# Performance work log

Measured on AMD Instinct MI355X. Metric: run time of the kernel, lower is better.

Reference implementation:

```python
import jax, jax.numpy as jnp
import numpy as np

B = 262144
P = 0.8
CLS_NUM_LIST = [500, 477, 456, 435, 415, 396, 378, 361, 345, 329, 314, 300, 286, 273, 261, 249, 238, 227, 217, 207, 197, 188, 180, 172, 164, 156, 149, 142, 136, 130, 124, 118, 113, 108, 103, 98, 94, 90, 85, 82, 78, 74, 71, 68, 65, 62, 59, 56, 54, 51, 49, 47, 45, 43, 41, 39, 37, 35, 34, 32, 31, 29, 28, 27, 26, 24, 23, 22, 21, 20, 19, 18, 18, 17, 16, 15, 15, 14, 13, 13, 12, 12, 11, 11, 10, 10, 9, 9, 8, 8, 8, 7, 7, 7, 6, 6, 6, 5, 5, 5]
C = len(CLS_NUM_LIST)


def _build_weight_matrix():
    n = np.asarray(CLS_NUM_LIST, dtype=np.float64).reshape(C, 1)
    wm = (1.0 / n) * n.T            # wm[i, j] = n_j / n_i
    wm[wm > 1] = 1.0
    wm = np.power(wm, P)
    return jnp.asarray(wm, dtype=jnp.float32)


def setup_inputs() -> dict:
    key = jax.random.key(0)
    kx, kt = jax.random.split(key)
    x = jax.random.normal(kx, (B, C), dtype=jnp.float32)
    target = jax.random.randint(kt, (B,), 0, C, dtype=jnp.int64)
    weight_matrix = _build_weight_matrix()                      # [C, C]
    neg_grad = jnp.full((1, C), 1e-06, dtype=jnp.float32)
    pos_grad = jnp.full((1, C), 1e-06, dtype=jnp.float32)
    return {"x": x, "target": target, "weight_matrix": weight_matrix,
            "neg_grad": neg_grad, "pos_grad": pos_grad}


def reference(x, target, weight_matrix, neg_grad, pos_grad):
    bs, num_classes = x.shape
    onehot = jax.nn.one_hot(target, num_classes, dtype=x.dtype)   # [B, C]
    # one_hot @ weight_matrix is algebraically a row gather
    weight = weight_matrix[target]                                # [B, C]
    weighted_x = x + jnp.log(weight)
    log_sm = jax.nn.log_softmax(weighted_x, axis=1)               # stable log(softmax)
    softmax_x = jnp.exp(log_sm)
    # grad-statistic accumulation (detached in the original)
    grad = jnp.abs(softmax_x - onehot)
    neg_grad_new = neg_grad + (grad * (1.0 - onehot)).sum(0)      # [1, C]
    pos_grad_new = pos_grad + (grad * onehot).sum(0)              # [1, C]
    ratio = pos_grad_new / neg_grad_new
    loss = -jnp.sum(onehot * log_sm) / bs
    return loss, neg_grad_new, pos_grad_new, ratio
```

## Files before the change

### kernel.cpp

```cpp
#include <hip/hip_runtime.h>

#define NCLS 100
#define NROWS 262144
#define MAIN_BLOCKS 2048
#define MAIN_THREADS 256
#define NWAVES (MAIN_THREADS / 64)
#define NOCT ((MAIN_BLOCKS * MAIN_THREADS) / 8)
#define ROWS_PER_OCT (NROWS / NOCT)
#define PART_LD MAIN_BLOCKS
#define NPC (2 * NCLS + 1)
#define WS_NEEDED ((size_t)NPC * PART_LD * 4)


#define LOADX(buf, rp) do {                                                    \
    buf[0] = (rp)[k];                                                          \
    buf[1] = (rp)[8 + k];                                                      \
    buf[2] = (rp)[16 + k];                                                     \
    buf[3] = (k == 0) ? (rp)[24] : make_float4(0.f, 0.f, 0.f, 0.f);            \
} while (0)

#define COMPROW(buf, LGT, VTX, TT) do {                                        \
    float4 e[4];                                                               \
    float sp = 0.f;                                                            \
    _Pragma("unroll")                                                          \
    for (int m = 0; m < 4; ++m) {                                              \
        if (8 * m + k < 25) {                                                  \
            e[m].x = __expf(buf[m].x + fminf(lgn[m].x - (LGT), 0.f));          \
            e[m].y = __expf(buf[m].y + fminf(lgn[m].y - (LGT), 0.f));          \
            e[m].z = __expf(buf[m].z + fminf(lgn[m].z - (LGT), 0.f));          \
            e[m].w = __expf(buf[m].w + fminf(lgn[m].w - (LGT), 0.f));          \
            sp += (e[m].x + e[m].y) + (e[m].z + e[m].w);                       \
        } else {                                                               \
            e[m] = make_float4(0.f, 0.f, 0.f, 0.f);                            \
        }                                                                      \
    }                                                                          \
    float s = sp + __shfl_xor(sp, 1, 64);                                      \
    s += __shfl_xor(s, 2, 64);                                                 \
    s += __shfl_xor(s, 4, 64);                                                 \
    const float inv_s = 1.0f / s;                                              \
    if (k == 0) {                                                              \
        loss_local += __logf(s) - (VTX);                                       \
        const float pt = __expf(VTX) * inv_s;                                  \
        atomicAdd(&lds_q[TT], pt);                                             \
        atomicAdd(&lds_pos[TT], 1.0f - pt);                                    \
    }                                                                          \
    _Pragma("unroll")                                                          \
    for (int m = 0; m < 4; ++m) {                                              \
        if (8 * m + k < 25) {                                                  \
            S4[m].x = fmaf(e[m].x, inv_s, S4[m].x);                            \
            S4[m].y = fmaf(e[m].y, inv_s, S4[m].y);                            \
            S4[m].z = fmaf(e[m].z, inv_s, S4[m].z);                            \
            S4[m].w = fmaf(e[m].w, inv_s, S4[m].w);                            \
        }                                                                      \
    }                                                                          \
} while (0)

__global__ __launch_bounds__(MAIN_THREADS, 4)
void seesaw_main(const float* __restrict__ x,
                 const int* __restrict__ target,
                 const float* __restrict__ wm,
                 float* __restrict__ part,
                 float* __restrict__ out,
                 int use_part) {
    __shared__ float lds_lgn[NCLS];
    __shared__ float lds_q[NCLS];
    __shared__ float lds_pos[NCLS];
    __shared__ float lds_S[NWAVES][NCLS];
    __shared__ float lds_loss[NWAVES];

    const int lane = threadIdx.x & 63;
    const int wave = threadIdx.x >> 6;
    const int k    = threadIdx.x & 7;
    const int oct  = (blockIdx.x * MAIN_THREADS + threadIdx.x) >> 3;

    int tr[ROWS_PER_OCT];
#pragma unroll
    for (int r = 0; r < ROWS_PER_OCT; ++r) tr[r] = target[oct + r * NOCT];

    if (threadIdx.x < NCLS) {
        lds_lgn[threadIdx.x] = __logf(wm[threadIdx.x]);
        lds_q[threadIdx.x] = 0.f;
        lds_pos[threadIdx.x] = 0.f;
    }
    __syncthreads();

    float vtx[ROWS_PER_OCT], lgt[ROWS_PER_OCT];
    const float4* xr[ROWS_PER_OCT];
#pragma unroll
    for (int r = 0; r < ROWS_PER_OCT; ++r) {
        const int row = oct + r * NOCT;
        xr[r] = reinterpret_cast<const float4*>(x + (size_t)row * NCLS);
        vtx[r] = x[(size_t)row * NCLS + tr[r]];
    }

    float4 lgn[4];
#pragma unroll
    for (int m = 0; m < 4; ++m) {
        const int g = 8 * m + k;
        if (g < 25) {
            lgn[m].x = lds_lgn[4 * g + 0];
            lgn[m].y = lds_lgn[4 * g + 1];
            lgn[m].z = lds_lgn[4 * g + 2];
            lgn[m].w = lds_lgn[4 * g + 3];
        } else {
            lgn[m] = make_float4(0.f, 0.f, 0.f, 0.f);
        }
    }
#pragma unroll
    for (int r = 0; r < ROWS_PER_OCT; ++r) lgt[r] = lds_lgn[tr[r]];

    float4 S4[4];
#pragma unroll
    for (int m = 0; m < 4; ++m) S4[m] = make_float4(0.f, 0.f, 0.f, 0.f);
    float loss_local = 0.0f;

    float4 xv0[4], xv1[4], xv2[4];
    LOADX(xv0, xr[0]);
    LOADX(xv1, xr[1]);
    LOADX(xv2, xr[2]);
    COMPROW(xv0, lgt[0], vtx[0], tr[0]);
    LOADX(xv0, xr[3]);
    COMPROW(xv1, lgt[1], vtx[1], tr[1]);
    COMPROW(xv2, lgt[2], vtx[2], tr[2]);
    COMPROW(xv0, lgt[3], vtx[3], tr[3]);

#pragma unroll
    for (int m = 0; m < 4; ++m) {
#pragma unroll
        for (int msk = 8; msk <= 32; msk <<= 1) {
            S4[m].x += __shfl_xor(S4[m].x, msk, 64);
            S4[m].y += __shfl_xor(S4[m].y, msk, 64);
            S4[m].z += __shfl_xor(S4[m].z, msk, 64);
            S4[m].w += __shfl_xor(S4[m].w, msk, 64);
        }
    }
#pragma unroll
    for (int msk = 1; msk < 64; msk <<= 1)
        loss_local += __shfl_xor(loss_local, msk, 64);
    if (lane == 0) lds_loss[wave] = loss_local;

    if (lane < 8) {
#pragma unroll
        for (int m = 0; m < 4; ++m) {
            const int g = 8 * m + lane;
            if (g < 25) {
                lds_S[wave][4 * g + 0] = S4[m].x;
                lds_S[wave][4 * g + 1] = S4[m].y;
                lds_S[wave][4 * g + 2] = S4[m].z;
                lds_S[wave][4 * g + 3] = S4[m].w;
            }
        }
    }
    __syncthreads();

    if (use_part) {
        if (threadIdx.x < NCLS) {
            const int j = threadIdx.x;
            float sb = 0.f;
#pragma unroll
            for (int w = 0; w < NWAVES; ++w) sb += lds_S[w][j];
            part[(size_t)j * PART_LD + blockIdx.x] = sb - lds_q[j];
            part[(size_t)(NCLS + j) * PART_LD + blockIdx.x] = lds_pos[j];
        }
        if (threadIdx.x == 0) {
            float l = 0.f;
#pragma unroll
            for (int w = 0; w < NWAVES; ++w) l += lds_loss[w];
            part[(size_t)(2 * NCLS) * PART_LD + blockIdx.x] = l;
        }
    } else {
        if (threadIdx.x < NCLS) {
            const int j = threadIdx.x;
            float sb = 0.f;
#pragma unroll
            for (int w = 0; w < NWAVES; ++w) sb += lds_S[w][j];
            atomicAdd(&out[1 + j], sb - lds_q[j]);
            atomicAdd(&out[1 + NCLS + j], lds_pos[j]);
        }
        if (threadIdx.x == 0) {
            float l = 0.f;
#pragma unroll
            for (int w = 0; w < NWAVES; ++w) l += lds_loss[w];
            atomicAdd(&out[0], l);
        }
    }
}

__global__ void seesaw_tail(const float* __restrict__ part,
                            const float* __restrict__ neg_in,
                            const float* __restrict__ pos_in,
                            float* __restrict__ out) {
    const int c = blockIdx.x;
    __shared__ float redn[NWAVES], redp[NWAVES];
    const int lane = threadIdx.x & 63;
    const int wave = threadIdx.x >> 6;

    float sn = 0.f, sp = 0.f;
    if (c < NCLS) {
        for (int b = threadIdx.x; b < PART_LD; b += MAIN_THREADS) {
            sn += part[(size_t)c * PART_LD + b];
            sp += part[(size_t)(NCLS + c) * PART_LD + b];
        }
    } else {
        for (int b = threadIdx.x; b < PART_LD; b += MAIN_THREADS)
            sn += part[(size_t)(2 * NCLS) * PART_LD + b];
    }
#pragma unroll
    for (int msk = 1; msk < 64; msk <<= 1) {
        sn += __shfl_xor(sn, msk, 64);
        sp += __shfl_xor(sp, msk, 64);
    }
    if (lane == 0) { redn[wave] = sn; redp[wave] = sp; }
    __syncthreads();
    if (threadIdx.x == 0) {
        float tn = 0.f, tp = 0.f;
#pragma unroll
        for (int w = 0; w < NWAVES; ++w) { tn += redn[w]; tp += redp[w]; }
        if (c < NCLS) {
            const float neg = neg_in[c] + tn;
            const float pos = pos_in[c] + tp;
            out[1 + c] = neg;
            out[1 + NCLS + c] = pos;
            out[1 + 2 * NCLS + c] = pos / neg;
        } else {
            out[0] = tn * (1.0f / (float)NROWS);
        }
    }
}

__global__ void seesaw_init(const float* __restrict__ neg_in,
                            const float* __restrict__ pos_in,
                            float* __restrict__ out) {
    int i = threadIdx.x;
    if (i == 0) out[0] = 0.0f;
    if (i < NCLS) {
        out[1 + i] = neg_in[i];
        out[1 + NCLS + i] = pos_in[i];
    }
}

__global__ void seesaw_fin(float* __restrict__ out) {
    int j = threadIdx.x;
    if (j == 0) out[0] *= (1.0f / (float)NROWS);
    if (j < NCLS) out[1 + 2 * NCLS + j] = out[1 + NCLS + j] / out[1 + j];
}

extern "C" void kernel_launch(void* const* d_in, const int* in_sizes, int n_in,
                              void* d_out, int out_size, void* d_ws, size_t ws_size,
                              hipStream_t stream) {
    const float* x      = (const float*)d_in[0];
    const int*   target = (const int*)d_in[1];
    const float* wm     = (const float*)d_in[2];
    const float* neg_in = (const float*)d_in[3];
    const float* pos_in = (const float*)d_in[4];
    float* out  = (float*)d_out;
    float* part = (float*)d_ws;

    if (ws_size >= WS_NEEDED) {
        hipLaunchKernelGGL(seesaw_main, dim3(MAIN_BLOCKS), dim3(MAIN_THREADS), 0, stream,
                           x, target, wm, part, out, 1);
        hipLaunchKernelGGL(seesaw_tail, dim3(NCLS + 1), dim3(MAIN_THREADS), 0, stream,
                           part, neg_in, pos_in, out);
    } else {
        hipLaunchKernelGGL(seesaw_init, dim3(1), dim3(256), 0, stream,
                           neg_in, pos_in, out);
        hipLaunchKernelGGL(seesaw_main, dim3(MAIN_BLOCKS), dim3(MAIN_THREADS), 0, stream,
                           x, target, wm, part, out, 0);
        hipLaunchKernelGGL(seesaw_fin, dim3(1), dim3(128), 0, stream, out);
    }
}
```

Before: 31.91 us.

## Stage contiguous x tiles through LDS with coalesced loads per block

Each block now owns a contiguous chunk of 128 rows. It copies them into LDS one 32-row tile at a time using fully coalesced float4 loads, then computes each row from LDS. The target-logit gather also reads from LDS instead of making a scattered global load. This is meant to replace strided per-octet row reads and the extra global gather, at the cost of serialising load and compute with block-wide barriers, so memory latency is no longer overlapped with compute within the block.

Measured after the change: 36.17 us. +13.3%, slower.

```diff
diff --git a/kernel.cpp b/kernel.cpp
--- a/kernel.cpp
+++ b/kernel.cpp
@@ -5,19 +5,13 @@
 #define MAIN_BLOCKS 2048
 #define MAIN_THREADS 256
 #define NWAVES (MAIN_THREADS / 64)
-#define NOCT ((MAIN_BLOCKS * MAIN_THREADS) / 8)
-#define ROWS_PER_OCT (NROWS / NOCT)
+#define TILE_ROWS 32
+#define NTILES 4
+#define TILE_F4 (TILE_ROWS * 25)
 #define PART_LD MAIN_BLOCKS
 #define NPC (2 * NCLS + 1)
 #define WS_NEEDED ((size_t)NPC * PART_LD * 4)
 
-
-#define LOADX(buf, rp) do {                                                    \
-    buf[0] = (rp)[k];                                                          \
-    buf[1] = (rp)[8 + k];                                                      \
-    buf[2] = (rp)[16 + k];                                                     \
-    buf[3] = (k == 0) ? (rp)[24] : make_float4(0.f, 0.f, 0.f, 0.f);            \
-} while (0)
 
 #define COMPROW(buf, LGT, VTX, TT) do {                                        \
     float4 e[4];                                                               \
@@ -55,6 +49,28 @@
     }                                                                          \
 } while (0)
 
+#define STAGE(TI) do {                                                         \
+    _Pragma("unroll")                                                          \
+    for (int i_ = 0; i_ < 4; ++i_) {                                           \
+        const int idx_ = i_ * MAIN_THREADS + threadIdx.x;                      \
+        if (idx_ < TILE_F4)                                                    \
+            lds_x4[idx_] = x4[base_f4 + (TI) * TILE_F4 + idx_];                \
+    }                                                                          \
+} while (0)
+
+#define COMPTILE(TI) do {                                                      \
+    const int t_ = tr[TI];                                                     \
+    const float lgt_ = lgt[TI];                                                \
+    float4 buf[4];                                                             \
+    buf[0] = lds_x4[oct * 25 + k];                                             \
+    buf[1] = lds_x4[oct * 25 + 8 + k];                                         \
+    buf[2] = lds_x4[oct * 25 + 16 + k];                                        \
+    buf[3] = (k == 0) ? lds_x4[oct * 25 + 24]                                  \
+                      : make_float4(0.f, 0.f, 0.f, 0.f);                       \
+    const float vt_ = lds_xs[oct * NCLS + t_];   \
+    COMPROW(buf, lgt_, vt_, t_);                                               \
+} while (0)
+
 __global__ __launch_bounds__(MAIN_THREADS, 4)
 void seesaw_main(const float* __restrict__ x,
                  const int* __restrict__ target,
@@ -62,6 +78,7 @@
                  float* __restrict__ part,
                  float* __restrict__ out,
                  int use_part) {
+    __shared__ float4 lds_x4[TILE_F4];
     __shared__ float lds_lgn[NCLS];
     __shared__ float lds_q[NCLS];
     __shared__ float lds_pos[NCLS];
@@ -71,27 +88,25 @@
     const int lane = threadIdx.x & 63;
     const int wave = threadIdx.x >> 6;
     const int k    = threadIdx.x & 7;
-    const int oct  = (blockIdx.x * MAIN_THREADS + threadIdx.x) >> 3;
-
-    int tr[ROWS_PER_OCT];
-#pragma unroll
-    for (int r = 0; r < ROWS_PER_OCT; ++r) tr[r] = target[oct + r * NOCT];
+    const int oct  = threadIdx.x >> 3;
+    const float* lds_xs = reinterpret_cast<const float*>(lds_x4);
+    const float4* x4 = reinterpret_cast<const float4*>(x);
+    const size_t base_f4 = (size_t)blockIdx.x * (NTILES * TILE_F4);
+    const int row0 = blockIdx.x * (NTILES * TILE_ROWS) + oct;
+
+    int tr[NTILES];
+    tr[0] = target[row0];
+    tr[1] = target[row0 + TILE_ROWS];
+    tr[2] = target[row0 + 2 * TILE_ROWS];
+    tr[3] = target[row0 + 3 * TILE_ROWS];
 
     if (threadIdx.x < NCLS) {
         lds_lgn[threadIdx.x] = __logf(wm[threadIdx.x]);
         lds_q[threadIdx.x] = 0.f;
         lds_pos[threadIdx.x] = 0.f;
     }
-    __syncthreads();
-
-    float vtx[ROWS_PER_OCT], lgt[ROWS_PER_OCT];
-    const float4* xr[ROWS_PER_OCT];
-#pragma unroll
-    for (int r = 0; r < ROWS_PER_OCT; ++r) {
-        const int row = oct + r * NOCT;
-        xr[r] = reinterpret_cast<const float4*>(x + (size_t)row * NCLS);
-        vtx[r] = x[(size_t)row * NCLS + tr[r]];
-    }
+    STAGE(0);
+    __syncthreads();
 
     float4 lgn[4];
 #pragma unroll
@@ -106,23 +121,30 @@
             lgn[m] = make_float4(0.f, 0.f, 0.f, 0.f);
         }
     }
-#pragma unroll
-    for (int r = 0; r < ROWS_PER_OCT; ++r) lgt[r] = lds_lgn[tr[r]];
+    float lgt[NTILES];
+    lgt[0] = lds_lgn[tr[0]];
+    lgt[1] = lds_lgn[tr[1]];
+    lgt[2] = lds_lgn[tr[2]];
+    lgt[3] = lds_lgn[tr[3]];
 
     float4 S4[4];
 #pragma unroll
     for (int m = 0; m < 4; ++m) S4[m] = make_float4(0.f, 0.f, 0.f, 0.f);
     float loss_local = 0.0f;
 
-    float4 xv0[4], xv1[4], xv2[4];
-    LOADX(xv0, xr[0]);
-    LOADX(xv1, xr[1]);
-    LOADX(xv2, xr[2]);
-    COMPROW(xv0, lgt[0], vtx[0], tr[0]);
-    LOADX(xv0, xr[3]);
-    COMPROW(xv1, lgt[1], vtx[1], tr[1]);
-    COMPROW(xv2, lgt[2], vtx[2], tr[2]);
-    COMPROW(xv0, lgt[3], vtx[3], tr[3]);
+    COMPTILE(0);
+    __syncthreads();
+    STAGE(1);
+    __syncthreads();
+    COMPTILE(1);
+    __syncthreads();
+    STAGE(2);
+    __syncthreads();
+    COMPTILE(2);
+    __syncthreads();
+    STAGE(3);
+    __syncthreads();
+    COMPTILE(3);
 
 #pragma unroll
     for (int m = 0; m < 4; ++m) {
```
